# Performance work log

Hardware: AMD Instinct MI355X
Metric: run time of the kernel (lower is better)

Reference implementation:

```python
import jax, jax.numpy as jnp
import numpy as np

N_SIN = 3  # fcn_n_sin (static)


def setup_inputs() -> dict:
    key = jax.random.key(0)
    ks = jax.random.split(key, 5)
    B, I, O, H = 256, 128, 128, 32
    F = 1 + 2 * N_SIN
    return {
        "x": jax.random.normal(ks[0], (B, I), dtype=jnp.float32),
        "W1": jax.random.normal(ks[1], (I, O, H, F), dtype=jnp.float32) * 0.3,
        "W2": jax.random.normal(ks[2], (I, O, 1, H), dtype=jnp.float32) * 0.3,
        "B1": jax.random.normal(ks[3], (I, O, H), dtype=jnp.float32) * 0.1,
        "B2": jax.random.normal(ks[4], (I, O, 1), dtype=jnp.float32) * 0.1,
    }


def reference(x, W1, W2, B1, B2):
    # x: [B, I]; per-(i,o) edge MLP on a scalar input, summed over i.
    omega = (2.0 ** jnp.arange(N_SIN)).astype(x.dtype)          # [S]
    ox = x[..., None] * omega                                    # [B, I, S]
    feat = jnp.concatenate([x[..., None], jnp.sin(ox), jnp.cos(ox)], axis=-1)  # [B, I, 1+2S]
    # First linear: per-edge [F -> H]
    h = jnp.einsum('bif,iohf->bioh', feat, W1) + B1              # [B, I, O, H]
    h = jax.nn.silu(h)
    # Second linear: per-edge [H -> 1], then sum over input dims i
    out = jnp.einsum('bioh,ioh->bio', h, W2[:, :, 0, :]) + B2[:, :, 0]  # [B, I, O]
    return out.sum(axis=1)                                       # [B, O]
```

## Files before the change

### kernel.cpp

```cpp
#include <hip/hip_runtime.h>
#include <hip/hip_bf16.h>

#define B_DIM 256
#define I_DIM 128
#define O_DIM 128
#define H_DIM 32
#define F_DIM 7
#define ICHUNK 8
#define NCHUNK (I_DIM / ICHUNK)
#define NLOG2E -1.4426950408889634f
#define NLN2   -0.6931471805599453f

typedef __attribute__((ext_vector_type(8))) short short8;
typedef __attribute__((ext_vector_type(4))) float float4v;

__device__ inline short bf16s(float v) {
    union { __hip_bfloat16 h; short s; } u;
    u.h = __float2bfloat16(v);
    return u.s;
}

__device__ inline float exp2_fast(float u) {
#if __has_builtin(__builtin_amdgcn_exp2f)
    return __builtin_amdgcn_exp2f(u);
#else
    return exp2f(u);
#endif
}

__device__ inline short8 feat_pack(float xv) {
    float s1 = __sinf(xv), c1 = __cosf(xv);
    float s2 = 2.f * s1 * c1, c2 = 1.f - 2.f * s1 * s1;
    float s4 = 2.f * s2 * c2, c4 = 1.f - 2.f * s2 * s2;
    short8 a;
    a[0] = bf16s(xv); a[1] = bf16s(s1); a[2] = bf16s(s2); a[3] = bf16s(s4);
    a[4] = bf16s(c1); a[5] = bf16s(c2); a[6] = bf16s(c4); a[7] = 0;
    return a;
}

__global__ __launch_bounds__(256)
void feat_kernel(const float* __restrict__ x, short* __restrict__ feat_g) {
    const int i = blockIdx.x;
    const int b = threadIdx.x;
    float xv = x[(size_t)b * I_DIM + i];
    *reinterpret_cast<short8*>(feat_g + ((size_t)i * B_DIM + b) * 8) = feat_pack(xv);
}

__global__ __launch_bounds__(256, 6)
void fcnkan_ws(const short* __restrict__ feat_g,
               const float* __restrict__ W1,
               const float* __restrict__ W2,
               const float* __restrict__ B1,
               const float* __restrict__ B2,
               float* __restrict__ ws) {
    __shared__ __align__(16) short w1_s[ICHUNK * H_DIM * 8];
    __shared__ float b1_s[ICHUNK * H_DIM];
    __shared__ float w2_s[ICHUNK * H_DIM];

    const int tid  = threadIdx.x;
    const int o    = blockIdx.x;
    const int ic0  = blockIdx.y * ICHUNK;
    const int w    = tid >> 6;
    const int lane = tid & 63;
    const int m    = lane & 15;
    const int q    = lane >> 4;

    const short8 zero8 = {};

    {
        int il = tid >> 5, h = tid & 31;
        size_t iobase = (size_t)(ic0 + il) * O_DIM + o;
        const float* wr = W1 + iobase * (H_DIM * F_DIM) + h * F_DIM;
        short8 bfr;
        #pragma unroll
        for (int f = 0; f < F_DIM; ++f) bfr[f] = bf16s(wr[f] * NLOG2E);
        bfr[7] = 0;
        *reinterpret_cast<short8*>(w1_s + tid * 8) = bfr;
        b1_s[tid] = B1[iobase * H_DIM + h] * NLOG2E;
        w2_s[tid] = W2[iobase * H_DIM + h] * NLN2;
    }
    __syncthreads();

    float acc[16];
    #pragma unroll
    for (int r = 0; r < 16; ++r) acc[r] = 0.f;

    #pragma unroll 1
    for (int il = 0; il < ICHUNK; ++il) {
        const short8* fG = reinterpret_cast<const short8*>(feat_g)
                           + (size_t)(ic0 + il) * B_DIM;
        const short8* wS = reinterpret_cast<const short8*>(w1_s) + il * H_DIM;

        short8 afrag[4];
        #pragma unroll
        for (int t = 0; t < 4; ++t)
            afrag[t] = fG[w * 64 + t * 16 + m];

        short8 bfrag[2];
        float  b1v[2], w2v[2];
        #pragma unroll
        for (int nt = 0; nt < 2; ++nt) {
            int h = nt * 16 + m;
            short8 b = wS[h];
            bfrag[nt] = (q == 0) ? b : zero8;
            b1v[nt] = b1_s[il * H_DIM + h];
            w2v[nt] = w2_s[il * H_DIM + h];
        }

        #pragma unroll
        for (int nt = 0; nt < 2; ++nt) {
            float4v c0 = {b1v[nt], b1v[nt], b1v[nt], b1v[nt]};
            #pragma unroll
            for (int t = 0; t < 4; ++t) {
                float4v z = __builtin_amdgcn_mfma_f32_16x16x32_bf16(
                    afrag[t], bfrag[nt], c0, 0, 0, 0);
                #pragma unroll
                for (int r = 0; r < 4; ++r) {
                    float u = z[r];
                    float e = exp2_fast(u);
                    float sg = __builtin_amdgcn_rcpf(1.f + e);
                    acc[t * 4 + r] = fmaf(u * sg, w2v[nt], acc[t * 4 + r]);
                }
            }
        }
    }

    #pragma unroll
    for (int r = 0; r < 16; ++r) {
        float v = acc[r];
        v += __shfl_xor(v, 1, 64);
        v += __shfl_xor(v, 2, 64);
        v += __shfl_xor(v, 4, 64);
        v += __shfl_xor(v, 8, 64);
        acc[r] = v;
    }

    float b2c = 0.f;
    for (int il = 0; il < ICHUNK; ++il) b2c += B2[(size_t)(ic0 + il) * O_DIM + o];

    if (m == 0) {
        float* wsp = ws + ((size_t)blockIdx.y * O_DIM + o) * B_DIM;
        #pragma unroll
        for (int t = 0; t < 4; ++t)
            #pragma unroll
            for (int r = 0; r < 4; ++r)
                wsp[w * 64 + t * 16 + q * 4 + r] = acc[t * 4 + r] + b2c;
    }
}

__global__ __launch_bounds__(256)
void reduce_kernel(const float* __restrict__ ws, float* __restrict__ out) {
    const int o = blockIdx.x;
    const int b = threadIdx.x;
    float s = 0.f;
    #pragma unroll
    for (int c = 0; c < NCHUNK; ++c)
        s += ws[((size_t)c * O_DIM + o) * B_DIM + b];
    out[(size_t)b * O_DIM + o] = s;
}

__global__ __launch_bounds__(256, 2)
void fcnkan_atomic(const float* __restrict__ x,
                   const float* __restrict__ W1,
                   const float* __restrict__ W2,
                   const float* __restrict__ B1,
                   const float* __restrict__ B2,
                   float* __restrict__ out) {
    __shared__ __align__(16) short feat_s[ICHUNK * B_DIM * 8];
    __shared__ __align__(16) short w1_s[ICHUNK * H_DIM * 8];
    __shared__ float b1_s[ICHUNK * H_DIM];
    __shared__ float w2_s[ICHUNK * H_DIM];

    const int tid  = threadIdx.x;
    const int o    = blockIdx.x;
    const int ic0  = blockIdx.y * ICHUNK;
    const int w    = tid >> 6;
    const int lane = tid & 63;
    const int m    = lane & 15;
    const int q    = lane >> 4;

    const short8 zero8 = {};

    {
        const float4* xp = reinterpret_cast<const float4*>(x + (size_t)tid * I_DIM + ic0);
        float4 x0 = xp[0], x1 = xp[1];
        float xr[8] = {x0.x, x0.y, x0.z, x0.w, x1.x, x1.y, x1.z, x1.w};
        #pragma unroll
        for (int il = 0; il < ICHUNK; ++il)
            *reinterpret_cast<short8*>(feat_s + (il * B_DIM + tid) * 8) = feat_pack(xr[il]);
    }
    {
        int il = tid >> 5, h = tid & 31;
        size_t iobase = (size_t)(ic0 + il) * O_DIM + o;
        const float* wr = W1 + iobase * (H_DIM * F_DIM) + h * F_DIM;
        short8 bfr;
        #pragma unroll
        for (int f = 0; f < F_DIM; ++f) bfr[f] = bf16s(wr[f]);
        bfr[7] = 0;
        *reinterpret_cast<short8*>(w1_s + tid * 8) = bfr;
        b1_s[tid] = B1[iobase * H_DIM + h];
        w2_s[tid] = W2[iobase * H_DIM + h];
    }
    __syncthreads();

    float acc[16];
    #pragma unroll
    for (int r = 0; r < 16; ++r) acc[r] = 0.f;

    #pragma unroll 1
    for (int il = 0; il < ICHUNK; ++il) {
        const short8* fS = reinterpret_cast<const short8*>(feat_s) + il * B_DIM;
        const short8* wS = reinterpret_cast<const short8*>(w1_s) + il * H_DIM;

        short8 afrag[4];
        #pragma unroll
        for (int t = 0; t < 4; ++t)
            afrag[t] = fS[w * 64 + t * 16 + m];

        short8 bfrag[2];
        float  b1v[2], w2v[2];
        #pragma unroll
        for (int nt = 0; nt < 2; ++nt) {
            int h = nt * 16 + m;
            short8 b = wS[h];
            bfrag[nt] = (q == 0) ? b : zero8;
            b1v[nt] = b1_s[il * H_DIM + h];
            w2v[nt] = w2_s[il * H_DIM + h];
        }

        #pragma unroll
        for (int nt = 0; nt < 2; ++nt) {
            float4v c0 = {b1v[nt], b1v[nt], b1v[nt], b1v[nt]};
            #pragma unroll
            for (int t = 0; t < 4; ++t) {
                float4v z = __builtin_amdgcn_mfma_f32_16x16x32_bf16(
                    afrag[t], bfrag[nt], c0, 0, 0, 0);
                #pragma unroll
                for (int r = 0; r < 4; ++r) {
                    float zz = z[r];
                    float sg = __builtin_amdgcn_rcpf(1.f + __expf(-zz));
                    acc[t * 4 + r] = fmaf(zz * sg, w2v[nt], acc[t * 4 + r]);
                }
            }
        }
    }

    #pragma unroll
    for (int r = 0; r < 16; ++r) {
        float v = acc[r];
        v += __shfl_xor(v, 1, 64);
        v += __shfl_xor(v, 2, 64);
        v += __shfl_xor(v, 4, 64);
        v += __shfl_xor(v, 8, 64);
        acc[r] = v;
    }

    float b2c = 0.f;
    for (int il = 0; il < ICHUNK; ++il) b2c += B2[(size_t)(ic0 + il) * O_DIM + o];

    if (m == 0) {
        #pragma unroll
        for (int t = 0; t < 4; ++t)
            #pragma unroll
            for (int r = 0; r < 4; ++r) {
                int b = w * 64 + t * 16 + q * 4 + r;
                atomicAdd(&out[(size_t)b * O_DIM + o], acc[t * 4 + r] + b2c);
            }
    }
}

extern "C" void kernel_launch(void* const* d_in, const int* in_sizes, int n_in,
                              void* d_out, int out_size, void* d_ws, size_t ws_size,
                              hipStream_t stream) {
    const float* x  = (const float*)d_in[0];
    const float* W1 = (const float*)d_in[1];
    const float* W2 = (const float*)d_in[2];
    const float* B1 = (const float*)d_in[3];
    const float* B2 = (const float*)d_in[4];
    float* out = (float*)d_out;
    float* ws  = (float*)d_ws;

    const size_t part_bytes = (size_t)NCHUNK * O_DIM * B_DIM * sizeof(float);
    const size_t feat_bytes = (size_t)I_DIM * B_DIM * 8 * sizeof(short);
    const size_t ws_need = part_bytes + feat_bytes;

    dim3 grid(O_DIM, NCHUNK);
    if (ws_size >= ws_need) {
        short* feat_g = (short*)((char*)d_ws + part_bytes);
        feat_kernel<<<I_DIM, B_DIM, 0, stream>>>(x, feat_g);
        fcnkan_ws<<<grid, 256, 0, stream>>>(feat_g, W1, W2, B1, B2, ws);
        reduce_kernel<<<O_DIM, B_DIM, 0, stream>>>(ws, out);
    } else {
        hipMemsetAsync(out, 0, (size_t)out_size * sizeof(float), stream);
        fcnkan_atomic<<<grid, 256, 0, stream>>>(x, W1, W2, B1, B2, out);
    }
}
```

Measured before the change: 105.7 us.

## Split batch across grid z with 128-thread blocks and packed float2 epilogue math

The main kernel now launches 128-thread blocks over a third grid dimension that splits the batch in two. Each block still stages the full weight chunk for its (o, i-chunk) into shared memory, so weight staging is repeated per batch half. The SiLU epilogue is rewritten with float2 vectors so the compiler can emit packed FP32 multiply and FMA instructions. The aim is more blocks and better latency hiding plus fewer VALU instructions, at the cost of duplicated weight loads and conversions.

```diff
diff --git a/kernel.cpp b/kernel.cpp
--- a/kernel.cpp
+++ b/kernel.cpp
@@ -13,6 +13,7 @@
 
 typedef __attribute__((ext_vector_type(8))) short short8;
 typedef __attribute__((ext_vector_type(4))) float float4v;
+typedef __attribute__((ext_vector_type(2))) float float2v;
 
 __device__ inline short bf16s(float v) {
     union { __hip_bfloat16 h; short s; } u;
@@ -46,7 +47,7 @@
     *reinterpret_cast<short8*>(feat_g + ((size_t)i * B_DIM + b) * 8) = feat_pack(xv);
 }
 
-__global__ __launch_bounds__(256, 6)
+__global__ __launch_bounds__(128, 7)
 void fcnkan_ws(const short* __restrict__ feat_g,
                const float* __restrict__ W1,
                const float* __restrict__ W2,
@@ -60,30 +61,34 @@
     const int tid  = threadIdx.x;
     const int o    = blockIdx.x;
     const int ic0  = blockIdx.y * ICHUNK;
+    const int bh   = blockIdx.z;
     const int w    = tid >> 6;
     const int lane = tid & 63;
     const int m    = lane & 15;
     const int q    = lane >> 4;
+    const int brow = bh * 128 + w * 64;
 
     const short8 zero8 = {};
 
-    {
-        int il = tid >> 5, h = tid & 31;
+    #pragma unroll
+    for (int s = 0; s < 2; ++s) {
+        int idx = s * 128 + tid;
+        int il = idx >> 5, h = idx & 31;
         size_t iobase = (size_t)(ic0 + il) * O_DIM + o;
         const float* wr = W1 + iobase * (H_DIM * F_DIM) + h * F_DIM;
         short8 bfr;
         #pragma unroll
         for (int f = 0; f < F_DIM; ++f) bfr[f] = bf16s(wr[f] * NLOG2E);
         bfr[7] = 0;
-        *reinterpret_cast<short8*>(w1_s + tid * 8) = bfr;
-        b1_s[tid] = B1[iobase * H_DIM + h] * NLOG2E;
-        w2_s[tid] = W2[iobase * H_DIM + h] * NLN2;
+        *reinterpret_cast<short8*>(w1_s + idx * 8) = bfr;
+        b1_s[idx] = B1[iobase * H_DIM + h] * NLOG2E;
+        w2_s[idx] = W2[iobase * H_DIM + h] * NLN2;
     }
     __syncthreads();
 
-    float acc[16];
-    #pragma unroll
-    for (int r = 0; r < 16; ++r) acc[r] = 0.f;
+    float2v acc2[8];
+    #pragma unroll
+    for (int p = 0; p < 8; ++p) acc2[p] = (float2v){0.f, 0.f};
 
     #pragma unroll 1
     for (int il = 0; il < ICHUNK; ++il) {
@@ -94,7 +99,7 @@
         short8 afrag[4];
         #pragma unroll
         for (int t = 0; t < 4; ++t)
-            afrag[t] = fG[w * 64 + t * 16 + m];
+            afrag[t] = fG[brow + t * 16 + m];
 
         short8 bfrag[2];
         float  b1v[2], w2v[2];
@@ -110,21 +115,34 @@
         #pragma unroll
         for (int nt = 0; nt < 2; ++nt) {
             float4v c0 = {b1v[nt], b1v[nt], b1v[nt], b1v[nt]};
+            float2v w2p = {w2v[nt], w2v[nt]};
             #pragma unroll
             for (int t = 0; t < 4; ++t) {
                 float4v z = __builtin_amdgcn_mfma_f32_16x16x32_bf16(
                     afrag[t], bfrag[nt], c0, 0, 0, 0);
                 #pragma unroll
-                for (int r = 0; r < 4; ++r) {
-                    float u = z[r];
-                    float e = exp2_fast(u);
-                    float sg = __builtin_amdgcn_rcpf(1.f + e);
-                    acc[t * 4 + r] = fmaf(u * sg, w2v[nt], acc[t * 4 + r]);
+                for (int r = 0; r < 4; r += 2) {
+                    float2v u = {z[r], z[r + 1]};
+                    float2v e = {exp2_fast(u.x), exp2_fast(u.y)};
+                    float2v d = u;
+                    float2v s = e + 1.f;
+                    float2v sg = {__builtin_amdgcn_rcpf(s.x),
+                                  __builtin_amdgcn_rcpf(s.y)};
+                    float2v p = d * sg;
+                    acc2[t * 2 + (r >> 1)] = p * w2p + acc2[t * 2 + (r >> 1)];
                 }
             }
         }
     }
 
+    float acc[16];
+    #pragma unroll
+    for (int t = 0; t < 4; ++t) {
+        acc[t * 4 + 0] = acc2[t * 2 + 0].x;
+        acc[t * 4 + 1] = acc2[t * 2 + 0].y;
+        acc[t * 4 + 2] = acc2[t * 2 + 1].x;
+        acc[t * 4 + 3] = acc2[t * 2 + 1].y;
+    }
     #pragma unroll
     for (int r = 0; r < 16; ++r) {
         float v = acc[r];
@@ -144,7 +162,7 @@
         for (int t = 0; t < 4; ++t)
             #pragma unroll
             for (int r = 0; r < 4; ++r)
-                wsp[w * 64 + t * 16 + q * 4 + r] = acc[t * 4 + r] + b2c;
+                wsp[brow + t * 16 + q * 4 + r] = acc[t * 4 + r] + b2c;
     }
 }
 
@@ -284,14 +302,15 @@
     const size_t feat_bytes = (size_t)I_DIM * B_DIM * 8 * sizeof(short);
     const size_t ws_need = part_bytes + feat_bytes;
 
-    dim3 grid(O_DIM, NCHUNK);
     if (ws_size >= ws_need) {
         short* feat_g = (short*)((char*)d_ws + part_bytes);
         feat_kernel<<<I_DIM, B_DIM, 0, stream>>>(x, feat_g);
-        fcnkan_ws<<<grid, 256, 0, stream>>>(feat_g, W1, W2, B1, B2, ws);
+        dim3 grid(O_DIM, NCHUNK, 2);
+        fcnkan_ws<<<grid, 128, 0, stream>>>(feat_g, W1, W2, B1, B2, ws);
         reduce_kernel<<<O_DIM, B_DIM, 0, stream>>>(ws, out);
     } else {
         hipMemsetAsync(out, 0, (size_t)out_size * sizeof(float), stream);
+        dim3 grid(O_DIM, NCHUNK);
         fcnkan_atomic<<<grid, 256, 0, stream>>>(x, W1, W2, B1, B2, out);
     }
 }
```

Measured after the change: 104.3 us. About the same (-1.3%).
